# Kernel optimization log

Hardware: AMD Instinct MI355X
Metric: run time of the kernel (lower is better)

Reference implementation:

```python
import jax, jax.numpy as jnp
import numpy as np
import math

B, NQ, NK, D, H = 4, 2048, 2048, 1024, 8
EPS = 1e-5


def _layernorm(x, g, b):
    mu = jnp.mean(x, axis=-1, keepdims=True)
    var = jnp.mean(jnp.square(x - mu), axis=-1, keepdims=True)
    return (x - mu) * jax.lax.rsqrt(var + EPS) * g + b


def setup_inputs() -> dict:
    key = jax.random.key(0)
    ks = jax.random.split(key, 12)
    s = 0.02
    return {
        "q": jax.random.normal(ks[0], (B, NQ, D), jnp.float32),
        "k": jax.random.normal(ks[1], (B, NK, D), jnp.float32),
        "v": jax.random.normal(ks[2], (B, NK, D), jnp.float32),
        "mask": jax.random.randint(ks[3], (B, NK), 0, 2).astype(bool),
        "Wq": jax.random.normal(ks[4], (D, D), jnp.float32) * s,
        "Wk": jax.random.normal(ks[5], (D, D), jnp.float32) * s,
        "Wv": jax.random.normal(ks[6], (D, D), jnp.float32) * s,
        "Wout": jax.random.normal(ks[7], (D, D), jnp.float32) * s,
        "bout": jnp.zeros((D,), jnp.float32),
        "g1": jnp.ones((D,), jnp.float32),
        "b1": jnp.zeros((D,), jnp.float32),
        "g2": jnp.ones((D,), jnp.float32),
        "b2": jnp.zeros((D,), jnp.float32),
    }


def reference(q, k, v, mask, Wq, Wk, Wv, Wout, bout, g1, b1, g2, b2):
    Dh = D // H
    qp = q @ Wq.T  # [B,NQ,D]
    kp = k @ Wk.T  # [B,NK,D]
    vp = v @ Wv.T  # [B,NK,D]
    # scatter: chunk last dim into H heads, cat along batch == reshape to heads
    qh = qp.reshape(B, NQ, H, Dh)
    kh = kp.reshape(B, NK, H, Dh)
    vh = vp.reshape(B, NK, H, Dh)
    # NOTE: original scales by sqrt(dim_out), not sqrt(head_dim)
    logits = jnp.einsum("bqhd,bkhd->bhqk", qh, kh) / math.sqrt(D)
    logits = jnp.where(mask[:, None, None, :], -jnp.inf, logits)
    A = jax.nn.softmax(logits, axis=-1)
    A = jnp.where(jnp.isnan(A), 0.0, A)  # rows fully masked -> 0
    att = jnp.einsum("bhqk,bkhd->bqhd", A, vh).reshape(B, NQ, D)
    out = _layernorm(qp + att, g1, b1)
    out = _layernorm(out + jax.nn.relu(out @ Wout.T + bout), g2, b2)
    return out
```

## Files before the change

### kernel.cpp

```cpp
#include <hip/hip_runtime.h>


typedef __attribute__((ext_vector_type(4))) float f32x4;
typedef __attribute__((ext_vector_type(16))) float f32x16;
typedef __attribute__((ext_vector_type(8))) short s16x8;
typedef __attribute__((ext_vector_type(4))) short s16x4;
typedef __attribute__((ext_vector_type(4))) unsigned int u32x4;

__device__ __forceinline__ unsigned short f2bf(float f) {
  union { float f; unsigned u; } x; x.f = f;
  unsigned r = x.u + 0x7fffu + ((x.u >> 16) & 1u);
  return (unsigned short)(r >> 16);
}
__device__ __forceinline__ float bf2f(unsigned short h) {
  union { unsigned u; float f; } x; x.u = ((unsigned)h) << 16;
  return x.f;
}

__device__ __forceinline__ void gload_lds16(const void* g, void* l) {
  __builtin_amdgcn_global_load_lds(
      (const __attribute__((address_space(1))) unsigned int*)g,
      (__attribute__((address_space(3))) unsigned int*)l, 16, 0, 0);
}

__device__ __forceinline__ unsigned lds_off(const void* p) {
  return (unsigned)(size_t)(const __attribute__((address_space(3))) void*)p;
}

__global__ __launch_bounds__(256) void cvt_fused(
    const float* __restrict__ q, const float* __restrict__ k,
    const float* __restrict__ v, const float* __restrict__ W0,
    const float* __restrict__ W1, const float* __restrict__ W2,
    const float* __restrict__ W3, unsigned short* __restrict__ qd,
    unsigned short* __restrict__ kd, unsigned short* __restrict__ vd,
    unsigned short* __restrict__ W0d, unsigned short* __restrict__ W1d,
    unsigned short* __restrict__ W2d, unsigned short* __restrict__ W3d,
    int n4big) {
  const int by = blockIdx.y;
  int i = blockIdx.x * blockDim.x + threadIdx.x;
  const float* s;
  unsigned short* d;
  if (by < 3) {
    if (i >= n4big) return;
    s = by == 0 ? q : by == 1 ? k : v;
    d = by == 0 ? qd : by == 1 ? kd : vd;
  } else {
    if (i >= 4 * 262144) return;
    const int wsel = i >> 18;
    s = wsel == 0 ? W0 : wsel == 1 ? W1 : wsel == 2 ? W2 : W3;
    d = wsel == 0 ? W0d : wsel == 1 ? W1d : wsel == 2 ? W2d : W3d;
    i &= 262143;
  }
  float4 f = reinterpret_cast<const float4*>(s)[i];
  s16x4 o;
  o[0] = (short)f2bf(f.x); o[1] = (short)f2bf(f.y);
  o[2] = (short)f2bf(f.z); o[3] = (short)f2bf(f.w);
  reinterpret_cast<s16x4*>(d)[i] = o;
}

__device__ __forceinline__ void xcd_tile(int wg, int& brow, int& bcol) {
  const int xcd = wg & 7, idx = wg >> 3;
  brow = ((xcd << 3) + (idx & 7)) * 128;
  bcol = (idx >> 3) * 128;
}

template<int RELU_BIAS>
__global__ __launch_bounds__(256) void gemm_bt(
    const unsigned short* __restrict__ A, const unsigned short* __restrict__ B,
    unsigned short* __restrict__ C, const float* __restrict__ bias,
    int M, int N, int K) {
  __shared__ __align__(16) unsigned short As[128 * 32];
  __shared__ __align__(16) unsigned short Bs[128 * 32];
  const int tid = threadIdx.x;
  const int lane = tid & 63;
  const int w = tid >> 6;
  int brow, bcol;
  xcd_tile(blockIdx.x + (blockIdx.y << 6), brow, bcol);
  const int wr = (w >> 1) * 64;
  const int wc = (w & 1) * 64;

  f32x4 acc[4][4] = {};

  const int srow = w * 32 + (lane >> 2);
  const int scol = (lane & 3) * 8;
  const int rfrag = lane & 15;
  const int kfrag = (lane >> 4) * 8;

  for (int k0 = 0; k0 < K; k0 += 32) {
    __syncthreads();
#pragma unroll
    for (int j = 0; j < 2; ++j) {
      const unsigned short* ga = A + (size_t)(brow + srow + j * 16) * K + k0 + scol;
      gload_lds16(ga, As + (w * 1024 + j * 512));
      const unsigned short* gb = B + (size_t)(bcol + srow + j * 16) * K + k0 + scol;
      gload_lds16(gb, Bs + (w * 1024 + j * 512));
    }
    asm volatile("s_waitcnt vmcnt(0)" ::: "memory");
    __syncthreads();
    s16x8 a[4], b[4];
#pragma unroll
    for (int m = 0; m < 4; ++m)
      a[m] = *(const s16x8*)(As + (wr + m * 16 + rfrag) * 32 + kfrag);
#pragma unroll
    for (int n = 0; n < 4; ++n)
      b[n] = *(const s16x8*)(Bs + (wc + n * 16 + rfrag) * 32 + kfrag);
#pragma unroll
    for (int m = 0; m < 4; ++m)
#pragma unroll
      for (int n = 0; n < 4; ++n)
        acc[m][n] = __builtin_amdgcn_mfma_f32_16x16x32_bf16(a[m], b[n], acc[m][n], 0, 0, 0);
  }

  const int crow = brow + wr + ((lane >> 4) * 4);
  const int ccol = bcol + wc + (lane & 15);
  float bv[4];
  if (RELU_BIAS) {
#pragma unroll
    for (int n = 0; n < 4; ++n) bv[n] = bias[ccol + n * 16];
  }
#pragma unroll
  for (int m = 0; m < 4; ++m)
#pragma unroll
    for (int n = 0; n < 4; ++n)
#pragma unroll
      for (int r = 0; r < 4; ++r) {
        float vv = acc[m][n][r];
        if (RELU_BIAS) vv = fmaxf(vv + bv[n], 0.f);
        C[(size_t)(crow + m * 16 + r) * N + ccol + n * 16] = f2bf(vv);
      }
}

__global__ __launch_bounds__(256) void gemm_proj3(
    const unsigned short* __restrict__ A0, const unsigned short* __restrict__ A1,
    const unsigned short* __restrict__ A2, const unsigned short* __restrict__ B0,
    const unsigned short* __restrict__ B1, const unsigned short* __restrict__ B2,
    unsigned short* __restrict__ C0, unsigned short* __restrict__ C1,
    unsigned short* __restrict__ C2, int M, int N, int K) {
  const int z = blockIdx.z;
  const unsigned short* __restrict__ A = z == 0 ? A0 : z == 1 ? A1 : A2;
  const unsigned short* __restrict__ B = z == 0 ? B0 : z == 1 ? B1 : B2;
  unsigned short* __restrict__ C = z == 0 ? C0 : z == 1 ? C1 : C2;

  __shared__ __align__(16) unsigned short As[128 * 32];
  __shared__ __align__(16) unsigned short Bs[128 * 32];
  const int tid = threadIdx.x;
  const int lane = tid & 63;
  const int w = tid >> 6;
  int brow, bcol;
  xcd_tile(blockIdx.x + (blockIdx.y << 6), brow, bcol);
  const int wr = (w >> 1) * 64;
  const int wc = (w & 1) * 64;

  f32x4 acc[4][4] = {};

  const int srow = w * 32 + (lane >> 2);
  const int scol = (lane & 3) * 8;
  const int rfrag = lane & 15;
  const int kfrag = (lane >> 4) * 8;

  for (int k0 = 0; k0 < K; k0 += 32) {
    __syncthreads();
#pragma unroll
    for (int j = 0; j < 2; ++j) {
      const unsigned short* ga = A + (size_t)(brow + srow + j * 16) * K + k0 + scol;
      gload_lds16(ga, As + (w * 1024 + j * 512));
      const unsigned short* gb = B + (size_t)(bcol + srow + j * 16) * K + k0 + scol;
      gload_lds16(gb, Bs + (w * 1024 + j * 512));
    }
    asm volatile("s_waitcnt vmcnt(0)" ::: "memory");
    __syncthreads();
    s16x8 a[4], b[4];
#pragma unroll
    for (int m = 0; m < 4; ++m)
      a[m] = *(const s16x8*)(As + (wr + m * 16 + rfrag) * 32 + kfrag);
#pragma unroll
    for (int n = 0; n < 4; ++n)
      b[n] = *(const s16x8*)(Bs + (wc + n * 16 + rfrag) * 32 + kfrag);
#pragma unroll
    for (int m = 0; m < 4; ++m)
#pragma unroll
      for (int n = 0; n < 4; ++n)
        acc[m][n] = __builtin_amdgcn_mfma_f32_16x16x32_bf16(a[m], b[n], acc[m][n], 0, 0, 0);
  }

  const int crow = brow + wr + ((lane >> 4) * 4);
  const int ccol = bcol + wc + (lane & 15);
#pragma unroll
  for (int m = 0; m < 4; ++m)
#pragma unroll
    for (int n = 0; n < 4; ++n)
#pragma unroll
      for (int r = 0; r < 4; ++r)
        C[(size_t)(crow + m * 16 + r) * N + ccol + n * 16] = f2bf(acc[m][n][r]);
}

__global__ __launch_bounds__(256, 2) void attn_fused(
    const unsigned short* __restrict__ Qp, const unsigned short* __restrict__ Kp,
    const unsigned short* __restrict__ Vp, const int* __restrict__ mask,
    unsigned short* __restrict__ Att) {
  constexpr int DD = 1024, NK = 2048;
  __shared__ __align__(16) unsigned short lds[16384];
  __shared__ __align__(16) float smaskF[2048];
  unsigned short* Ks = lds;
  unsigned short* Vs = lds + 8192;

  const int tid = threadIdx.x, lane = tid & 63, w = tid >> 6;
  const int quad = lane >> 4, lq = lane & 15;
  const int hi = lane >> 5, q5 = lane & 31;
  const int L = blockIdx.x;
  const int bh = (L & 7) * 4 + (L >> 7);
  const int qt = (L >> 3) & 15;
  const int b = bh >> 3, h = bh & 7;
  const int q0 = qt * 128;
  const unsigned short* Qbase = Qp + ((size_t)b * 2048 + q0) * DD + h * 128;
  const unsigned short* Kbase = Kp + (size_t)b * 2048 * DD + h * 128;
  const unsigned short* Vbase = Vp + (size_t)b * 2048 * DD + h * 128;

#pragma unroll
  for (int j = 0; j < 8; ++j) {
    int row = w * 32 + j * 4 + quad;
    const unsigned short* g = Qbase + (size_t)row * DD + lq * 8;
    gload_lds16(g, lds + w * 4096 + j * 512);
  }
  asm volatile("s_waitcnt vmcnt(0)" ::: "memory");
  __syncthreads();
  s16x8 qf[8];
#pragma unroll
  for (int ds = 0; ds < 8; ++ds)
    qf[ds] = *(const s16x8*)(lds + (w * 32 + q5) * 128 + ds * 16 + hi * 8);

  {
    const int4* mp = (const int4*)(mask + b * NK);
    int4 m0 = mp[tid];
    int4 m1 = mp[tid + 256];
    f32x4 w0, w1;
    w0[0] = m0.x ? -1e30f : 0.f; w0[1] = m0.y ? -1e30f : 0.f;
    w0[2] = m0.z ? -1e30f : 0.f; w0[3] = m0.w ? -1e30f : 0.f;
    w1[0] = m1.x ? -1e30f : 0.f; w1[1] = m1.y ? -1e30f : 0.f;
    w1[2] = m1.z ? -1e30f : 0.f; w1[3] = m1.w ? -1e30f : 0.f;
    *(f32x4*)(smaskF + 4 * tid) = w0;
    *(f32x4*)(smaskF + 4 * (tid + 256)) = w1;
  }

  const unsigned vb0 = lds_off(Vs);
  const int swzq = (q5 & 7) << 4;

  f32x16 o[4] = {};
  float mrow = -1e30f, lrow = 0.f;

  for (int kt = 0; kt < NK / 64; ++kt) {
    const int k0 = kt * 64;
    __syncthreads();
#pragma unroll
    for (int j = 0; j < 4; ++j) {
      int row = w * 16 + j * 4 + quad;
      int cb = lq * 16;
      int cbs = cb ^ ((row & 7) << 4);
      const unsigned short* g = Kbase + (size_t)(k0 + row) * DD + (cbs >> 1);
      gload_lds16(g, Ks + w * 2048 + j * 512);
    }
#pragma unroll
    for (int it = 0; it < 4; ++it) {
      int s = w * 256 + it * 64 + lane;
      int kk = ((s >> 6) << 2) | ((s >> 1) & 3);
      int dd = (((s >> 3) & 7) << 4) | ((s & 1) << 3);
      const unsigned short* g = Vbase + (size_t)(k0 + kk) * DD + dd;
      gload_lds16(g, Vs + (size_t)(w * 256 + it * 64) * 8);
    }
    asm volatile("s_waitcnt vmcnt(0)" ::: "memory");
    __syncthreads();

    f32x16 acc0 = {}, acc1 = {};
    __builtin_amdgcn_s_setprio(1);
#pragma unroll
    for (int ds = 0; ds < 8; ++ds) {
      int cbs = (ds * 32 + hi * 16) ^ swzq;
      s16x8 kf0 = *(const s16x8*)((const char*)Ks + q5 * 256 + cbs);
      s16x8 kf1 = *(const s16x8*)((const char*)Ks + (q5 + 32) * 256 + cbs);
      acc0 = __builtin_amdgcn_mfma_f32_32x32x16_bf16(kf0, qf[ds], acc0, 0, 0, 0);
      acc1 = __builtin_amdgcn_mfma_f32_32x32x16_bf16(kf1, qf[ds], acc1, 0, 0, 0);
    }
    __builtin_amdgcn_s_setprio(0);

    float sv0[16], sv1[16];
#pragma unroll
    for (int g2 = 0; g2 < 4; ++g2) {
      f32x4 m0 = *(const f32x4*)(smaskF + k0 + g2 * 8 + hi * 4);
      f32x4 m1 = *(const f32x4*)(smaskF + k0 + 32 + g2 * 8 + hi * 4);
#pragma unroll
      for (int j2 = 0; j2 < 4; ++j2) {
        sv0[g2 * 4 + j2] = fmaf(acc0[g2 * 4 + j2], 0.03125f, m0[j2]);
        sv1[g2 * 4 + j2] = fmaf(acc1[g2 * 4 + j2], 0.03125f, m1[j2]);
      }
    }

    float tm = fmaxf(sv0[0], sv1[0]);
#pragma unroll
    for (int r = 1; r < 16; ++r) tm = fmaxf(tm, fmaxf(sv0[r], sv1[r]));
    tm = fmaxf(tm, __shfl_xor(tm, 32, 64));
    const bool up = !__all(tm - mrow <= 8.f);
    float al = 1.f;
    if (up) {
      float mn = fmaxf(mrow, tm);
      al = __expf(mrow - mn);
      mrow = mn;
    }
    float rs = 0.f;
    s16x8 pa[4];
    auto packP = [&](const float (&sv)[16], s16x8* paOut) {
      float p[16];
#pragma unroll
      for (int r = 0; r < 16; ++r) {
        p[r] = __expf(sv[r] - mrow);
        rs += p[r];
      }
#pragma unroll
      for (int i2 = 0; i2 < 2; ++i2) {
        unsigned a0, b0, a1, b1;
        asm("v_cvt_pk_bf16_f32 %0, %1, %2" : "=v"(a0) : "v"(p[i2 * 8 + 0]), "v"(p[i2 * 8 + 1]));
        asm("v_cvt_pk_bf16_f32 %0, %1, %2" : "=v"(b0) : "v"(p[i2 * 8 + 4]), "v"(p[i2 * 8 + 5]));
        asm("v_cvt_pk_bf16_f32 %0, %1, %2" : "=v"(a1) : "v"(p[i2 * 8 + 2]), "v"(p[i2 * 8 + 3]));
        asm("v_cvt_pk_bf16_f32 %0, %1, %2" : "=v"(b1) : "v"(p[i2 * 8 + 6]), "v"(p[i2 * 8 + 7]));
        asm volatile("v_permlane32_swap_b32 %0, %1" : "+v"(a0), "+v"(b0));
        asm volatile("v_permlane32_swap_b32 %0, %1" : "+v"(a1), "+v"(b1));
        u32x4 wv;
        wv[0] = a0; wv[1] = a1; wv[2] = b0; wv[3] = b1;
        paOut[i2] = *(s16x8*)&wv;
      }
    };
    packP(sv0, &pa[0]);
    packP(sv1, &pa[2]);
    rs += __shfl_xor(rs, 32, 64);
    lrow = lrow * al + rs;
    if (up) {
#pragma unroll
      for (int reg = 0; reg < 16; ++reg) {
        float alo = __shfl(al, (reg & 3) + 8 * (reg >> 2) + 4 * hi, 64);
#pragma unroll
        for (int db = 0; db < 4; ++db) o[db][reg] *= alo;
      }
    }

#pragma unroll
    for (int db = 0; db < 4; ++db) {
      s16x4 vlo[4], vhi[4];
#pragma unroll
      for (int kb2 = 0; kb2 < 4; ++kb2) {
        const unsigned va = vb0 + (kb2 * 4 + hi * 2) * 1024 +
                            (db * 2 + (quad & 1)) * 128 + lq * 8;
        asm volatile("ds_read_b64_tr_b16 %0, %2\n\t"
                     "ds_read_b64_tr_b16 %1, %2 offset:1024"
                     : "=&v"(vlo[kb2]), "=&v"(vhi[kb2])
                     : "v"(va)
                     : "memory");
      }
      asm volatile("s_waitcnt lgkmcnt(0)" ::: "memory");
      __builtin_amdgcn_sched_barrier(0);
      __builtin_amdgcn_s_setprio(1);
#pragma unroll
      for (int kb2 = 0; kb2 < 4; ++kb2) {
        s16x8 vv;
#pragma unroll
        for (int j = 0; j < 4; ++j) { vv[j] = vlo[kb2][j]; vv[4 + j] = vhi[kb2][j]; }
        o[db] = __builtin_amdgcn_mfma_f32_32x32x16_bf16(pa[kb2], vv, o[db], 0, 0, 0);
      }
      __builtin_amdgcn_s_setprio(0);
    }
  }

  float inv = (mrow <= -1e29f || lrow <= 0.f) ? 0.f : 1.f / lrow;
#pragma unroll
  for (int reg = 0; reg < 16; ++reg) {
    const int rown = (reg & 3) + 8 * (reg >> 2) + 4 * hi;
    float invo = __shfl(inv, rown, 64);
    const int q = q0 + w * 32 + rown;
#pragma unroll
    for (int db = 0; db < 4; ++db) {
      Att[((size_t)b * 2048 + q) * DD + h * 128 + db * 32 + q5] =
          f2bf(o[db][reg] * invo);
    }
  }
}

template<int OUT_F32>
__global__ __launch_bounds__(256) void add_ln(
    const unsigned short* __restrict__ X, const unsigned short* __restrict__ Y,
    const float* __restrict__ gam, const float* __restrict__ bet,
    void* __restrict__ out) {
  const int row = blockIdx.x;
  const int tid = threadIdx.x;
  const int lane = tid & 63, w = tid >> 6;
  __shared__ float rbuf[8];
  const size_t base = (size_t)row * 1024 + tid * 4;
  s16x4 xa = *(const s16x4*)(X + base);
  s16x4 yb = *(const s16x4*)(Y + base);
  float x[4];
  float s1 = 0.f, s2 = 0.f;
#pragma unroll
  for (int j = 0; j < 4; ++j) {
    x[j] = bf2f((unsigned short)xa[j]) + bf2f((unsigned short)yb[j]);
    s1 += x[j];
    s2 += x[j] * x[j];
  }
#pragma unroll
  for (int d = 1; d < 64; d <<= 1) {
    s1 += __shfl_xor(s1, d, 64);
    s2 += __shfl_xor(s2, d, 64);
  }
  if (lane == 0) { rbuf[w] = s1; rbuf[4 + w] = s2; }
  __syncthreads();
  float t1 = rbuf[0] + rbuf[1] + rbuf[2] + rbuf[3];
  float t2 = rbuf[4] + rbuf[5] + rbuf[6] + rbuf[7];
  float mu = t1 * (1.f / 1024.f);
  float var = t2 * (1.f / 1024.f) - mu * mu;
  float rstd = rsqrtf(fmaxf(var, 0.f) + 1e-5f);
  float4 g4 = *(const float4*)(gam + tid * 4);
  float4 b4 = *(const float4*)(bet + tid * 4);
  float gg[4] = {g4.x, g4.y, g4.z, g4.w};
  float bb[4] = {b4.x, b4.y, b4.z, b4.w};
  if (OUT_F32) {
    float4 o4;
    o4.x = (x[0] - mu) * rstd * gg[0] + bb[0];
    o4.y = (x[1] - mu) * rstd * gg[1] + bb[1];
    o4.z = (x[2] - mu) * rstd * gg[2] + bb[2];
    o4.w = (x[3] - mu) * rstd * gg[3] + bb[3];
    *(float4*)((float*)out + base) = o4;
  } else {
    s16x4 o;
#pragma unroll
    for (int j = 0; j < 4; ++j)
      o[j] = (short)f2bf((x[j] - mu) * rstd * gg[j] + bb[j]);
    *(s16x4*)((unsigned short*)out + base) = o;
  }
}

extern "C" void kernel_launch(void* const* d_in, const int* in_sizes, int n_in,
                              void* d_out, int out_size, void* d_ws, size_t ws_size,
                              hipStream_t stream) {
  const float* q  = (const float*)d_in[0];
  const float* k  = (const float*)d_in[1];
  const float* v  = (const float*)d_in[2];
  const int* msk  = (const int*)d_in[3];
  const float* Wq = (const float*)d_in[4];
  const float* Wk = (const float*)d_in[5];
  const float* Wv = (const float*)d_in[6];
  const float* Wo = (const float*)d_in[7];
  const float* bo = (const float*)d_in[8];
  const float* g1 = (const float*)d_in[9];
  const float* b1 = (const float*)d_in[10];
  const float* g2 = (const float*)d_in[11];
  const float* b2 = (const float*)d_in[12];
  float* out = (float*)d_out;

  char* ws = (char*)d_ws;
  const size_t S = (size_t)8192 * 1024 * 2;
  unsigned short* qb  = (unsigned short*)(ws + 0 * S);
  unsigned short* kb  = (unsigned short*)(ws + 1 * S);
  unsigned short* vb  = (unsigned short*)(ws + 2 * S);
  unsigned short* qpb = (unsigned short*)(ws + 3 * S);
  unsigned short* kpb = (unsigned short*)(ws + 4 * S);
  unsigned short* vpb = (unsigned short*)(ws + 5 * S);
  unsigned short* attb = qb;
  unsigned short* h1b  = kb;
  unsigned short* h2b  = vb;
  unsigned short* Wqb = (unsigned short*)(ws + 6 * S);
  unsigned short* Wkb = Wqb + (size_t)1024 * 1024;
  unsigned short* Wvb = Wkb + (size_t)1024 * 1024;
  unsigned short* Wob = Wvb + (size_t)1024 * 1024;

  const int n4big = 8192 * 1024 / 4;
  cvt_fused<<<dim3(8192, 4), 256, 0, stream>>>(
      q, k, v, Wq, Wk, Wv, Wo, qb, kb, vb, Wqb, Wkb, Wvb, Wob, n4big);

  gemm_proj3<<<dim3(64, 8, 3), 256, 0, stream>>>(
      qb, kb, vb, Wqb, Wkb, Wvb, qpb, kpb, vpb, 8192, 1024, 1024);

  attn_fused<<<512, 256, 0, stream>>>(qpb, kpb, vpb, msk, attb);

  add_ln<0><<<8192, 256, 0, stream>>>(qpb, attb, g1, b1, (void*)h1b);
  gemm_bt<1><<<dim3(64, 8), 256, 0, stream>>>(h1b, Wob, h2b, bo, 8192, 1024, 1024);
  add_ln<1><<<8192, 256, 0, stream>>>(h1b, h2b, g2, b2, (void*)out);
}
```

Baseline: 235.3 us.

## Fuse fp32-to-bf16 activation conversion into the QKV projection GEMM

The q/k/v activations are no longer converted to bf16 in a separate pass. The projection GEMM now loads fp32 tiles straight into LDS with an XOR swizzle and converts them to bf16 with packed conversion instructions while building the MFMA fragments. Only the weights still go through a standalone conversion kernel. This removes one full read and write of the large activation tensors, at the cost of twice the LDS footprint and global traffic for the A tile, plus extra conversion ALU work in the GEMM inner loop.

```diff
diff --git a/kernel.cpp b/kernel.cpp
--- a/kernel.cpp
+++ b/kernel.cpp
@@ -27,30 +27,16 @@
   return (unsigned)(size_t)(const __attribute__((address_space(3))) void*)p;
 }
 
-__global__ __launch_bounds__(256) void cvt_fused(
-    const float* __restrict__ q, const float* __restrict__ k,
-    const float* __restrict__ v, const float* __restrict__ W0,
-    const float* __restrict__ W1, const float* __restrict__ W2,
-    const float* __restrict__ W3, unsigned short* __restrict__ qd,
-    unsigned short* __restrict__ kd, unsigned short* __restrict__ vd,
+__global__ __launch_bounds__(256) void cvt_w(
+    const float* __restrict__ W0, const float* __restrict__ W1,
+    const float* __restrict__ W2, const float* __restrict__ W3,
     unsigned short* __restrict__ W0d, unsigned short* __restrict__ W1d,
-    unsigned short* __restrict__ W2d, unsigned short* __restrict__ W3d,
-    int n4big) {
-  const int by = blockIdx.y;
+    unsigned short* __restrict__ W2d, unsigned short* __restrict__ W3d) {
   int i = blockIdx.x * blockDim.x + threadIdx.x;
-  const float* s;
-  unsigned short* d;
-  if (by < 3) {
-    if (i >= n4big) return;
-    s = by == 0 ? q : by == 1 ? k : v;
-    d = by == 0 ? qd : by == 1 ? kd : vd;
-  } else {
-    if (i >= 4 * 262144) return;
-    const int wsel = i >> 18;
-    s = wsel == 0 ? W0 : wsel == 1 ? W1 : wsel == 2 ? W2 : W3;
-    d = wsel == 0 ? W0d : wsel == 1 ? W1d : wsel == 2 ? W2d : W3d;
-    i &= 262143;
-  }
+  const int wsel = i >> 18;
+  const float* s = wsel == 0 ? W0 : wsel == 1 ? W1 : wsel == 2 ? W2 : W3;
+  unsigned short* d = wsel == 0 ? W0d : wsel == 1 ? W1d : wsel == 2 ? W2d : W3d;
+  i &= 262143;
   float4 f = reinterpret_cast<const float4*>(s)[i];
   s16x4 o;
   o[0] = (short)f2bf(f.x); o[1] = (short)f2bf(f.y);
@@ -131,17 +117,17 @@
 }
 
 __global__ __launch_bounds__(256) void gemm_proj3(
-    const unsigned short* __restrict__ A0, const unsigned short* __restrict__ A1,
-    const unsigned short* __restrict__ A2, const unsigned short* __restrict__ B0,
+    const float* __restrict__ A0, const float* __restrict__ A1,
+    const float* __restrict__ A2, const unsigned short* __restrict__ B0,
     const unsigned short* __restrict__ B1, const unsigned short* __restrict__ B2,
     unsigned short* __restrict__ C0, unsigned short* __restrict__ C1,
     unsigned short* __restrict__ C2, int M, int N, int K) {
   const int z = blockIdx.z;
-  const unsigned short* __restrict__ A = z == 0 ? A0 : z == 1 ? A1 : A2;
+  const float* __restrict__ A = z == 0 ? A0 : z == 1 ? A1 : A2;
   const unsigned short* __restrict__ B = z == 0 ? B0 : z == 1 ? B1 : B2;
   unsigned short* __restrict__ C = z == 0 ? C0 : z == 1 ? C1 : C2;
 
-  __shared__ __align__(16) unsigned short As[128 * 32];
+  __shared__ __align__(16) float Asf[128 * 32];
   __shared__ __align__(16) unsigned short Bs[128 * 32];
   const int tid = threadIdx.x;
   const int lane = tid & 63;
@@ -155,27 +141,46 @@
 
   const int srow = w * 32 + (lane >> 2);
   const int scol = (lane & 3) * 8;
+  const int arow = w * 32 + (lane >> 3);
+  const int acb = (lane & 7) * 16;
   const int rfrag = lane & 15;
-  const int kfrag = (lane >> 4) * 8;
+  const int quad = lane >> 4;
 
   for (int k0 = 0; k0 < K; k0 += 32) {
     __syncthreads();
 #pragma unroll
     for (int j = 0; j < 2; ++j) {
-      const unsigned short* ga = A + (size_t)(brow + srow + j * 16) * K + k0 + scol;
-      gload_lds16(ga, As + (w * 1024 + j * 512));
       const unsigned short* gb = B + (size_t)(bcol + srow + j * 16) * K + k0 + scol;
       gload_lds16(gb, Bs + (w * 1024 + j * 512));
     }
+#pragma unroll
+    for (int j = 0; j < 4; ++j) {
+      int row = arow + j * 8;
+      int cbs = acb ^ ((row & 7) << 4);
+      const float* ga = A + (size_t)(brow + row) * K + k0 + (cbs >> 2);
+      gload_lds16(ga, (char*)Asf + w * 4096 + j * 1024);
+    }
     asm volatile("s_waitcnt vmcnt(0)" ::: "memory");
     __syncthreads();
     s16x8 a[4], b[4];
 #pragma unroll
-    for (int m = 0; m < 4; ++m)
-      a[m] = *(const s16x8*)(As + (wr + m * 16 + rfrag) * 32 + kfrag);
+    for (int m = 0; m < 4; ++m) {
+      const int r = wr + m * 16 + rfrag;
+      const int b1 = (quad * 32) ^ ((r & 7) << 4);
+      const int b2 = (quad * 32 + 16) ^ ((r & 7) << 4);
+      f32x4 a0 = *(const f32x4*)((const char*)Asf + r * 128 + b1);
+      f32x4 a1 = *(const f32x4*)((const char*)Asf + r * 128 + b2);
+      unsigned w0, w1, w2, w3;
+      asm("v_cvt_pk_bf16_f32 %0, %1, %2" : "=v"(w0) : "v"(a0[0]), "v"(a0[1]));
+      asm("v_cvt_pk_bf16_f32 %0, %1, %2" : "=v"(w1) : "v"(a0[2]), "v"(a0[3]));
+      asm("v_cvt_pk_bf16_f32 %0, %1, %2" : "=v"(w2) : "v"(a1[0]), "v"(a1[1]));
+      asm("v_cvt_pk_bf16_f32 %0, %1, %2" : "=v"(w3) : "v"(a1[2]), "v"(a1[3]));
+      u32x4 wv; wv[0] = w0; wv[1] = w1; wv[2] = w2; wv[3] = w3;
+      a[m] = *(s16x8*)&wv;
+    }
 #pragma unroll
     for (int n = 0; n < 4; ++n)
-      b[n] = *(const s16x8*)(Bs + (wc + n * 16 + rfrag) * 32 + kfrag);
+      b[n] = *(const s16x8*)(Bs + (wc + n * 16 + rfrag) * 32 + quad * 8);
 #pragma unroll
     for (int m = 0; m < 4; ++m)
 #pragma unroll
@@ -183,8 +188,8 @@
         acc[m][n] = __builtin_amdgcn_mfma_f32_16x16x32_bf16(a[m], b[n], acc[m][n], 0, 0, 0);
   }
 
-  const int crow = brow + wr + ((lane >> 4) * 4);
-  const int ccol = bcol + wc + (lane & 15);
+  const int crow = brow + wr + (quad * 4);
+  const int ccol = bcol + wc + rfrag;
 #pragma unroll
   for (int m = 0; m < 4; ++m)
 #pragma unroll
@@ -454,26 +459,21 @@
 
   char* ws = (char*)d_ws;
   const size_t S = (size_t)8192 * 1024 * 2;
-  unsigned short* qb  = (unsigned short*)(ws + 0 * S);
-  unsigned short* kb  = (unsigned short*)(ws + 1 * S);
-  unsigned short* vb  = (unsigned short*)(ws + 2 * S);
   unsigned short* qpb = (unsigned short*)(ws + 3 * S);
   unsigned short* kpb = (unsigned short*)(ws + 4 * S);
   unsigned short* vpb = (unsigned short*)(ws + 5 * S);
-  unsigned short* attb = qb;
-  unsigned short* h1b  = kb;
-  unsigned short* h2b  = vb;
+  unsigned short* attb = (unsigned short*)(ws + 0 * S);
+  unsigned short* h1b  = (unsigned short*)(ws + 1 * S);
+  unsigned short* h2b  = (unsigned short*)(ws + 2 * S);
   unsigned short* Wqb = (unsigned short*)(ws + 6 * S);
   unsigned short* Wkb = Wqb + (size_t)1024 * 1024;
   unsigned short* Wvb = Wkb + (size_t)1024 * 1024;
   unsigned short* Wob = Wvb + (size_t)1024 * 1024;
 
-  const int n4big = 8192 * 1024 / 4;
-  cvt_fused<<<dim3(8192, 4), 256, 0, stream>>>(
-      q, k, v, Wq, Wk, Wv, Wo, qb, kb, vb, Wqb, Wkb, Wvb, Wob, n4big);
+  cvt_w<<<4096, 256, 0, stream>>>(Wq, Wk, Wv, Wo, Wqb, Wkb, Wvb, Wob);
 
   gemm_proj3<<<dim3(64, 8, 3), 256, 0, stream>>>(
-      qb, kb, vb, Wqb, Wkb, Wvb, qpb, kpb, vpb, 8192, 1024, 1024);
+      q, k, v, Wqb, Wkb, Wvb, qpb, kpb, vpb, 8192, 1024, 1024);
 
   attn_fused<<<512, 256, 0, stream>>>(qpb, kpb, vpb, msk, attb);
 
```

After: 228.8 us (median of 3 runs). 2.8% less time.
